# Optimization experiments

Hardware: AMD Instinct MI355X
Metric: run time of the kernel (lower is better)

## Reference

```python
import jax, jax.numpy as jnp
import numpy as np

RGB2GRAY = jnp.array([0.299, 0.587, 0.114], dtype=jnp.float32)

H_IMG, W_IMG = 1080, 1920
NUM, GRID_Y, GRID_X, GRID_W = 1, 16, 16, 8


def _identity_grids(num, grid_y, grid_x, grid_w):
    ident = jnp.array([1., 0, 0, 0, 0, 1., 0, 0, 0, 0, 1., 0], dtype=jnp.float32)
    return jnp.broadcast_to(ident, (num, grid_y, grid_x, grid_w, 12))


def setup_inputs() -> dict:
    key = jax.random.key(0)
    k1, k2 = jax.random.split(key)
    rgb = jax.random.uniform(k1, (3, H_IMG, W_IMG), dtype=jnp.float32)
    # learned grids = identity affine + small perturbation (so slicing is non-trivial)
    grids = _identity_grids(NUM, GRID_Y, GRID_X, GRID_W) \
        + 0.05 * jax.random.normal(k2, (NUM, GRID_Y, GRID_X, GRID_W, 12), dtype=jnp.float32)
    return {"rgb": rgb, "grids": grids, "idx": 0}


def _bilateral_slice(grid, guidance):
    """Trilinear slice. grid: (Hg, Wg, L, 12); guidance: (Hi, Wi) in [0,1].
    Returns (Hi, Wi, 12)."""
    Hg, Wg, L, _ = grid.shape
    Hi, Wi = guidance.shape
    # align_corners-style pixel -> grid coords
    gy = jnp.linspace(0.0, Hg - 1.0, Hi, dtype=jnp.float32)[:, None]   # (Hi,1)
    gx = jnp.linspace(0.0, Wg - 1.0, Wi, dtype=jnp.float32)[None, :]   # (1,Wi)
    gz = jnp.clip(guidance, 0.0, 1.0) * (L - 1.0)                      # (Hi,Wi)

    fy = jnp.floor(gy); wy = gy - fy
    fx = jnp.floor(gx); wx = gx - fx
    fz = jnp.floor(gz); wz = gz - fz
    y0 = jnp.clip(fy.astype(jnp.int32), 0, Hg - 1); y1 = jnp.clip(y0 + 1, 0, Hg - 1)
    x0 = jnp.clip(fx.astype(jnp.int32), 0, Wg - 1); x1 = jnp.clip(x0 + 1, 0, Wg - 1)
    z0 = jnp.clip(fz.astype(jnp.int32), 0, L - 1);  z1 = jnp.clip(z0 + 1, 0, L - 1)

    out = jnp.zeros((Hi, Wi, 12), dtype=grid.dtype)
    for yi, wyi in ((y0, 1.0 - wy), (y1, wy)):
        for xi, wxi in ((x0, 1.0 - wx), (x1, wx)):
            for zi, wzi in ((z0, 1.0 - wz), (z1, wz)):
                w = (wyi * wxi * wzi)[..., None]          # (Hi,Wi,1)
                out = out + grid[yi, xi, zi] * w          # gather -> (Hi,Wi,12)
    return out


def reference(rgb, grids, idx):
    grid = grids[idx]                         # (Hg, Wg, L, 12)
    rgb_hwc = jnp.transpose(rgb, (1, 2, 0))   # (H, W, 3)
    gray = jnp.tensordot(rgb_hwc, RGB2GRAY, axes=([-1], [0]))  # (H, W)
    affine = _bilateral_slice(grid, gray)     # (H, W, 12)
    affine_mat = affine.reshape(-1, 3, 4)     # (H*W, 3, 4)
    rgb_flat = rgb_hwc.reshape(-1, 3)         # (H*W, 3)
    res_rgb = jnp.einsum('nij,nj->ni', affine_mat[..., :3], rgb_flat) + affine_mat[..., 3]
    return (affine_mat, res_rgb)
```

## Files before the change

### kernel.cpp

```cpp
#include <hip/hip_runtime.h>

#define H_IMG 1080
#define W_IMG 1920
#define HW_PIX (H_IMG * W_IMG)
#define GY 16
#define GX 16
#define GL 8
#define CF 12
#define SEG 192

__global__ __launch_bounds__(192) void bg_kernel(
    const float* __restrict__ rgb,
    const float* __restrict__ grids,
    const int* __restrict__ idxp,
    float* __restrict__ out)
{
    __shared__ float4 sg[96];

    const int tid = threadIdx.x;
    const int y = blockIdx.y;
    const int xbase = blockIdx.x * SEG;

    const float* grid = grids + (size_t)idxp[0] * (GY * GX * GL * CF);

    float gyv = (float)y * (15.0f / 1079.0f);
    float fy = floorf(gyv);
    float wy = gyv - fy;
    int y0 = min(max((int)fy, 0), GY - 1);
    int y1 = min(y0 + 1, GY - 1);

    int xc0 = (int)floorf((float)xbase * (15.0f / 1919.0f));

    if (tid < 96) {
        int xi  = tid / 24;
        int rem = tid - xi * 24;
        int z   = rem / 3;
        int c4  = rem - z * 3;
        int xc  = min(xc0 + xi, GX - 1);
        const float4* c0 = (const float4*)(grid + (size_t)((y0 * GX + xc) * GL + z) * CF) + c4;
        const float4* c1 = (const float4*)(grid + (size_t)((y1 * GX + xc) * GL + z) * CF) + c4;
        float4 a = *c0, b = *c1;
        float wy0 = 1.0f - wy;
        float4 r;
        r.x = wy0 * a.x + wy * b.x;
        r.y = wy0 * a.y + wy * b.y;
        r.z = wy0 * a.z + wy * b.z;
        r.w = wy0 * a.w + wy * b.w;
        sg[tid] = r;
    }
    __syncthreads();

    const int x = xbase + tid;
    const int p = y * W_IMG + x;

    float r = rgb[p];
    float g = rgb[HW_PIX + p];
    float b = rgb[2 * HW_PIX + p];

    float gray = 0.299f * r + 0.587f * g + 0.114f * b;

    float gxv = (float)x * (15.0f / 1919.0f);
    float fx = floorf(gxv), wx = gxv - fx;
    float gz = fminf(fmaxf(gray, 0.0f), 1.0f) * 7.0f;
    float fz = floorf(gz), wz = gz - fz;

    int x0g = min(max((int)fx, 0), GX - 1);
    int x1g = min(x0g + 1, GX - 1);
    int xi0 = x0g - xc0;
    int xi1 = x1g - xc0;
    int z0 = min(max((int)fz, 0), GL - 1);
    int z1 = min(z0 + 1, GL - 1);

    float w00 = (1.0f - wx) * (1.0f - wz);
    float w01 = (1.0f - wx) * wz;
    float w10 = wx * (1.0f - wz);
    float w11 = wx * wz;

    const float4* A = sg + (xi0 * 24 + z0 * 3);
    const float4* B = sg + (xi0 * 24 + z1 * 3);
    const float4* C = sg + (xi1 * 24 + z0 * 3);
    const float4* D = sg + (xi1 * 24 + z1 * 3);

    float4 acc[3];
#pragma unroll
    for (int j = 0; j < 3; ++j) {
        float4 va = A[j], vb = B[j], vc = C[j], vd = D[j];
        float4 o;
        o.x = fmaf(w00, va.x, fmaf(w01, vb.x, fmaf(w10, vc.x, w11 * vd.x)));
        o.y = fmaf(w00, va.y, fmaf(w01, vb.y, fmaf(w10, vc.y, w11 * vd.y)));
        o.z = fmaf(w00, va.z, fmaf(w01, vb.z, fmaf(w10, vc.z, w11 * vd.z)));
        o.w = fmaf(w00, va.w, fmaf(w01, vb.w, fmaf(w10, vc.w, w11 * vd.w)));
        acc[j] = o;
    }

    float4* ao = (float4*)out + (size_t)p * 3;
    ao[0] = acc[0];
    ao[1] = acc[1];
    ao[2] = acc[2];

    float res0 = fmaf(acc[0].x, r, fmaf(acc[0].y, g, fmaf(acc[0].z, b, acc[0].w)));
    float res1 = fmaf(acc[1].x, r, fmaf(acc[1].y, g, fmaf(acc[1].z, b, acc[1].w)));
    float res2 = fmaf(acc[2].x, r, fmaf(acc[2].y, g, fmaf(acc[2].z, b, acc[2].w)));

    float* ro = out + (size_t)HW_PIX * 12 + (size_t)p * 3;
    ro[0] = res0;
    ro[1] = res1;
    ro[2] = res2;
}

extern "C" void kernel_launch(void* const* d_in, const int* in_sizes, int n_in,
                              void* d_out, int out_size, void* d_ws, size_t ws_size,
                              hipStream_t stream) {
    const float* rgb   = (const float*)d_in[0];
    const float* grids = (const float*)d_in[1];
    const int*   idx   = (const int*)d_in[2];
    float*       out   = (float*)d_out;

    dim3 grid(W_IMG / SEG, H_IMG);
    dim3 block(SEG);
    bg_kernel<<<grid, block, 0, stream>>>(rgb, grids, idx, out);
}
```

Before: 154.1 us.

## Stage input and output through shared memory for coalesced vector global access

After: 146.4 us. -5.0%, faster.

```diff
diff --git a/kernel.cpp b/kernel.cpp
--- a/kernel.cpp
+++ b/kernel.cpp
@@ -16,10 +16,21 @@
     float* __restrict__ out)
 {
     __shared__ float4 sg[96];
+    __shared__ float  s_in[3 * SEG];
+    __shared__ float  s_aff[SEG * 12];
+    __shared__ float  s_res[SEG * 3];
 
     const int tid = threadIdx.x;
     const int y = blockIdx.y;
     const int xbase = blockIdx.x * SEG;
+    const int p0 = y * W_IMG + xbase;
+
+    if (tid < 144) {
+        const int ch = tid / 48;
+        const int i  = tid - ch * 48;
+        ((float4*)s_in)[ch * 48 + i] =
+            ((const float4*)(rgb + (size_t)ch * HW_PIX + p0))[i];
+    }
 
     const float* grid = grids + (size_t)idxp[0] * (GY * GX * GL * CF);
 
@@ -41,21 +52,20 @@
         const float4* c1 = (const float4*)(grid + (size_t)((y1 * GX + xc) * GL + z) * CF) + c4;
         float4 a = *c0, b = *c1;
         float wy0 = 1.0f - wy;
-        float4 r;
-        r.x = wy0 * a.x + wy * b.x;
-        r.y = wy0 * a.y + wy * b.y;
-        r.z = wy0 * a.z + wy * b.z;
-        r.w = wy0 * a.w + wy * b.w;
-        sg[tid] = r;
+        float4 rr;
+        rr.x = wy0 * a.x + wy * b.x;
+        rr.y = wy0 * a.y + wy * b.y;
+        rr.z = wy0 * a.z + wy * b.z;
+        rr.w = wy0 * a.w + wy * b.w;
+        sg[tid] = rr;
     }
     __syncthreads();
 
     const int x = xbase + tid;
-    const int p = y * W_IMG + x;
 
-    float r = rgb[p];
-    float g = rgb[HW_PIX + p];
-    float b = rgb[2 * HW_PIX + p];
+    float r = s_in[tid];
+    float g = s_in[SEG + tid];
+    float b = s_in[2 * SEG + tid];
 
     float gray = 0.299f * r + 0.587f * g + 0.114f * b;
 
@@ -93,19 +103,27 @@
         acc[j] = o;
     }
 
-    float4* ao = (float4*)out + (size_t)p * 3;
-    ao[0] = acc[0];
-    ao[1] = acc[1];
-    ao[2] = acc[2];
+    float4* sa = (float4*)(s_aff + tid * 12);
+    sa[0] = acc[0];
+    sa[1] = acc[1];
+    sa[2] = acc[2];
 
-    float res0 = fmaf(acc[0].x, r, fmaf(acc[0].y, g, fmaf(acc[0].z, b, acc[0].w)));
-    float res1 = fmaf(acc[1].x, r, fmaf(acc[1].y, g, fmaf(acc[1].z, b, acc[1].w)));
-    float res2 = fmaf(acc[2].x, r, fmaf(acc[2].y, g, fmaf(acc[2].z, b, acc[2].w)));
+    s_res[tid * 3 + 0] = fmaf(acc[0].x, r, fmaf(acc[0].y, g, fmaf(acc[0].z, b, acc[0].w)));
+    s_res[tid * 3 + 1] = fmaf(acc[1].x, r, fmaf(acc[1].y, g, fmaf(acc[1].z, b, acc[1].w)));
+    s_res[tid * 3 + 2] = fmaf(acc[2].x, r, fmaf(acc[2].y, g, fmaf(acc[2].z, b, acc[2].w)));
 
-    float* ro = out + (size_t)HW_PIX * 12 + (size_t)p * 3;
-    ro[0] = res0;
-    ro[1] = res1;
-    ro[2] = res2;
+    __syncthreads();
+
+    const float4* sa4 = (const float4*)s_aff;
+    float4* ao = (float4*)(out + (size_t)p0 * 12);
+    ao[tid]           = sa4[tid];
+    ao[tid + SEG]     = sa4[tid + SEG];
+    ao[tid + 2 * SEG] = sa4[tid + 2 * SEG];
+
+    if (tid < 144) {
+        ((float4*)(out + (size_t)HW_PIX * 12 + (size_t)p0 * 3))[tid] =
+            ((const float4*)s_res)[tid];
+    }
 }
 
 extern "C" void kernel_launch(void* const* d_in, const int* in_sizes, int n_in,
```
